# Kernel tuning notes

Measured on AMD Instinct MI355X. Metric: run time of the kernel, lower is better.

## Reference

```python
import jax, jax.numpy as jnp
import numpy as np

NI, ND, NH = 64, 64, 4
NB, NLOC, NNEI = 4, 2048, 64


def setup_inputs() -> dict:
    key = jax.random.key(0)
    ks = jax.random.split(key, 7)
    g1 = jax.random.normal(ks[0], (NB, NLOC, NI), dtype=jnp.float32)
    gg1 = jax.random.normal(ks[1], (NB, NLOC, NNEI, NI), dtype=jnp.float32)
    nlist_mask = jax.random.randint(ks[2], (NB, NLOC, NNEI), 0, 2).astype(bool)
    # torch Linear weight (out, in); store transposed for x @ W
    Wq = jax.random.normal(ks[3], (NI, ND * NH), dtype=jnp.float32) * (1.0 / np.sqrt(NI))
    Wkv = jax.random.normal(ks[4], (NI, (ND + NI) * NH), dtype=jnp.float32) * (1.0 / np.sqrt(NI))
    Wh = jax.random.normal(ks[5], (NI * NH, NI), dtype=jnp.float32) * (1.0 / np.sqrt(NI * NH))
    bh = jax.random.normal(ks[6], (NI,), dtype=jnp.float32) * 0.01
    return {"g1": g1, "gg1": gg1, "nlist_mask": nlist_mask,
            "Wq": Wq, "Wkv": Wkv, "Wh": Wh, "bh": bh}


def reference(g1, gg1, nlist_mask, Wq, Wkv, Wh, bh):
    nb, nloc, nnei = nlist_mask.shape
    ni, nd, nh = NI, ND, NH
    # q: (nb, nloc, nh, nd)
    q = (g1 @ Wq).reshape(nb, nloc, nd, nh).transpose(0, 1, 3, 2)
    # kv: (nb, nloc, nnei, nd, 2*nh) -> (nb, nloc, 2*nh, nnei, nd); valid since ni == nd
    kv = (gg1 @ Wkv).reshape(nb, nloc, nnei, nd, 2 * nh).transpose(0, 1, 4, 2, 3)
    k = kv[:, :, :nh]          # (nb, nloc, nh, nnei, nd)
    v = kv[:, :, nh:2 * nh]    # (nb, nloc, nh, nnei, nd)
    attnw = jnp.einsum('blhd,blhjd->blhj', q, k) / np.sqrt(nd).astype(np.float32)
    m = nlist_mask[:, :, None, :]  # (nb, nloc, 1, nnei)
    attnw = jnp.where(m, attnw, -jnp.inf)
    attnw = jax.nn.softmax(attnw, axis=-1)
    attnw = jnp.where(m, attnw, 0.0)
    ret = jnp.einsum('blhj,blhjd->blhd', attnw, v).reshape(nb, nloc, nh * ni)
    return ret @ Wh + bh
```

## Files before the change

kernel.cpp:

```cpp
#include <hip/hip_runtime.h>
#include <hip/hip_fp16.h>
#include <math.h>

#define NATOM 8192

namespace {

typedef _Float16 half8 __attribute__((ext_vector_type(8)));
typedef _Float16 half2t __attribute__((ext_vector_type(2)));
typedef float f32x4 __attribute__((ext_vector_type(4)));

__global__ void pack_weights(const float* __restrict__ Wkv,
                             const float* __restrict__ Wq,
                             const float* __restrict__ Wh,
                             _Float16* __restrict__ out) {
  int tid = blockIdx.x * 256 + threadIdx.x;
  if (tid < 32768) {
    int i = tid >> 9, c = tid & 511;
    int ks = i >> 5, jj = i & 7, lqk = (i >> 3) & 3;
    int d = c >> 3, e = c & 7, isv = e >> 2, h = e & 3;
    int T = isv * 16 + (d >> 2);
    int m = ((d & 3) << 2) | h;
    int l = lqk * 16 + m;
    out[(((T * 2 + ks) * 64) + l) * 8 + jj] = (_Float16)Wkv[i * 512 + c];
  } else if (tid < 49152) {
    int idx = tid - 32768;
    int i = idx >> 8, c = idx & 255;
    out[32768 + c * 64 + i] = (_Float16)Wq[i * 256 + c];
  } else {
    int idx = tid - 49152;
    int k = idx >> 6, c = idx & 63;
    out[49152 + c * 256 + k] = (_Float16)Wh[k * 64 + c];
  }
}

__device__ __forceinline__ float dot8(half8 a, half8 b, float acc) {
  acc = __builtin_amdgcn_fdot2((half2t){a[0], a[1]}, (half2t){b[0], b[1]}, acc, false);
  acc = __builtin_amdgcn_fdot2((half2t){a[2], a[3]}, (half2t){b[2], b[3]}, acc, false);
  acc = __builtin_amdgcn_fdot2((half2t){a[4], a[5]}, (half2t){b[4], b[5]}, acc, false);
  acc = __builtin_amdgcn_fdot2((half2t){a[6], a[7]}, (half2t){b[6], b[7]}, acc, false);
  return acc;
}

__global__ __launch_bounds__(256, 4)
void local_atten_kernel(const float* __restrict__ g1,
                        const float* __restrict__ gg1,
                        const int* __restrict__ mask,
                        const _Float16* __restrict__ wpack,
                        const float* __restrict__ bh,
                        float* __restrict__ out) {
  __shared__ __align__(16) __half gs[64 * 64];
  __shared__ __align__(16) __half g1h[64];
  __shared__ __align__(16) unsigned char blob[3072];
  __shared__ __align__(8) __half aws2[64][4];
  __shared__ __align__(16) __half rets[256];

  float* qs = reinterpret_cast<float*>(blob);
  __half (*sred)[4][64] = reinterpret_cast<__half(*)[4][64]>(blob + 1024);
  float (*redbuf)[64] = reinterpret_cast<float(*)[64]>(blob);

  const _Float16* wkvp = wpack;
  const _Float16* wqp  = wpack + 32768;
  const _Float16* whp  = wpack + 49152;

  const int t = threadIdx.x;
  const int lane = t & 63;
  const int wave = t >> 6;
  const int lq = lane >> 4;
  const int lr = lane & 15;
  const int atom = blockIdx.x;

  if (t < 64) g1h[t] = __float2half(g1[(size_t)atom * 64 + t]);

  {
    const float4* src = reinterpret_cast<const float4*>(gg1 + (size_t)atom * 4096);
#pragma unroll
    for (int r = 0; r < 4; ++r) {
      int idx4 = t + 256 * r;
      int j = idx4 >> 4;
      int i4 = (idx4 & 15) << 2;
      float4 v = src[idx4];
      __half2 h01 = __floats2half2_rn(v.x, v.y);
      __half2 h23 = __floats2half2_rn(v.z, v.w);
      int g = i4 >> 3;
      int addr = j * 64 + ((g ^ (j & 7)) << 3) + (i4 & 7);
      union { __half2 h[2]; uint2 u; } pk;
      pk.h[0] = h01; pk.h[1] = h23;
      *reinterpret_cast<uint2*>(&gs[addr]) = pk.u;
    }
  }
  __syncthreads();

  half8 bfrag[4][2];
  {
    const __half* bp0 = &gs[lr * 64 + ((lq ^ (lr & 7)) << 3)];
    const __half* bp1 = &gs[lr * 64 + (((4 + lq) ^ (lr & 7)) << 3)];
#pragma unroll
    for (int jt = 0; jt < 4; ++jt) {
      bfrag[jt][0] = *reinterpret_cast<const half8*>(bp0 + jt * 1024);
      bfrag[jt][1] = *reinterpret_cast<const half8*>(bp1 + jt * 1024);
    }
  }

  const half8* ap_base = reinterpret_cast<const half8*>(wkvp);
  half8 a0 = ap_base[(wave * 4) * 128 + lane];
  half8 a1 = ap_base[(wave * 4) * 128 + 64 + lane];

  {
    float qacc = 0.f;
    const half8* wrow = reinterpret_cast<const half8*>(wqp + t * 64);
    const half8* grow = reinterpret_cast<const half8*>(&g1h[0]);
#pragma unroll
    for (int ks = 0; ks < 8; ++ks) qacc = dot8(wrow[ks], grow[ks], qacc);
    qs[t] = qacc;
  }
  __syncthreads();

  float sacc[4][4];
#pragma unroll
  for (int jt = 0; jt < 4; ++jt)
#pragma unroll
    for (int h = 0; h < 4; ++h) sacc[jt][h] = 0.f;

#pragma unroll
  for (int it = 0; it < 4; ++it) {
    const int T = wave * 4 + it;
    const int Tn = (it < 3) ? (T + 1) : (16 + wave * 4);
    half8 na0 = ap_base[Tn * 128 + lane];
    half8 na1 = ap_base[Tn * 128 + 64 + lane];

    const int d = T * 4 + lq;
    float4 q4 = *reinterpret_cast<const float4*>(&qs[d * 4]);
#pragma unroll
    for (int jt = 0; jt < 4; ++jt) {
      f32x4 acc = {0.f, 0.f, 0.f, 0.f};
      acc = __builtin_amdgcn_mfma_f32_16x16x32_f16(a0, bfrag[jt][0], acc, 0, 0, 0);
      acc = __builtin_amdgcn_mfma_f32_16x16x32_f16(a1, bfrag[jt][1], acc, 0, 0, 0);
      sacc[jt][0] = fmaf(acc[0], q4.x, sacc[jt][0]);
      sacc[jt][1] = fmaf(acc[1], q4.y, sacc[jt][1]);
      sacc[jt][2] = fmaf(acc[2], q4.z, sacc[jt][2]);
      sacc[jt][3] = fmaf(acc[3], q4.w, sacc[jt][3]);
    }
    a0 = na0; a1 = na1;
  }

  const int mreg = mask[(size_t)atom * 64 + lane];

#pragma unroll
  for (int jt = 0; jt < 4; ++jt)
#pragma unroll
    for (int h = 0; h < 4; ++h) {
      sacc[jt][h] += __shfl_xor(sacc[jt][h], 16);
      sacc[jt][h] += __shfl_xor(sacc[jt][h], 32);
    }
  if (lq == 0) {
#pragma unroll
    for (int h = 0; h < 4; ++h)
#pragma unroll
      for (int jt = 0; jt < 4; ++jt)
        sred[wave][h][jt * 16 + lr] = __float2half(sacc[jt][h]);
  }
  __syncthreads();

  {
    float s = __half2float(sred[0][wave][lane]) + __half2float(sred[1][wave][lane]) +
              __half2float(sred[2][wave][lane]) + __half2float(sred[3][wave][lane]);
    s *= 0.125f;
    s = mreg ? s : -INFINITY;
    float mx = s;
#pragma unroll
    for (int off = 32; off > 0; off >>= 1) mx = fmaxf(mx, __shfl_xor(mx, off));
    float pe = mreg ? __expf(s - mx) : 0.f;
    float sum = pe;
#pragma unroll
    for (int off = 32; off > 0; off >>= 1) sum += __shfl_xor(sum, off);
    float aw = (sum > 0.f) ? (pe / sum) : 0.f;
    aws2[lane][wave] = __float2half(aw);
  }
  __syncthreads();

  float awf[4][4];
#pragma unroll
  for (int jt = 0; jt < 4; ++jt) {
    union { uint2 u; __half2 h[2]; } awu;
    awu.u = *reinterpret_cast<const uint2*>(&aws2[jt * 16 + lr][0]);
    float2 f01 = __half22float2(awu.h[0]);
    float2 f23 = __half22float2(awu.h[1]);
    awf[jt][0] = f01.x; awf[jt][1] = f01.y; awf[jt][2] = f23.x; awf[jt][3] = f23.y;
  }

#pragma unroll
  for (int it = 0; it < 4; ++it) {
    const int T = 16 + wave * 4 + it;
    half8 na0 = a0, na1 = a1;
    if (it < 3) {
      na0 = ap_base[(T + 1) * 128 + lane];
      na1 = ap_base[(T + 1) * 128 + 64 + lane];
    }
    float part[4] = {0.f, 0.f, 0.f, 0.f};
#pragma unroll
    for (int jt = 0; jt < 4; ++jt) {
      f32x4 acc = {0.f, 0.f, 0.f, 0.f};
      acc = __builtin_amdgcn_mfma_f32_16x16x32_f16(a0, bfrag[jt][0], acc, 0, 0, 0);
      acc = __builtin_amdgcn_mfma_f32_16x16x32_f16(a1, bfrag[jt][1], acc, 0, 0, 0);
      part[0] = fmaf(acc[0], awf[jt][0], part[0]);
      part[1] = fmaf(acc[1], awf[jt][1], part[1]);
      part[2] = fmaf(acc[2], awf[jt][2], part[2]);
      part[3] = fmaf(acc[3], awf[jt][3], part[3]);
    }
#pragma unroll
    for (int r = 0; r < 4; ++r) {
      part[r] += __shfl_xor(part[r], 1);
      part[r] += __shfl_xor(part[r], 2);
      part[r] += __shfl_xor(part[r], 4);
      part[r] += __shfl_xor(part[r], 8);
    }
    if (lr == 0) {
      const int d = (T - 16) * 4 + lq;
#pragma unroll
      for (int r = 0; r < 4; ++r) rets[r * 64 + d] = __float2half(part[r]);
    }
    a0 = na0; a1 = na1;
  }
  __syncthreads();

  {
    float part = 0.f;
    const half8* wrow = reinterpret_cast<const half8*>(whp + lane * 256 + wave * 64);
    const half8* rrow = reinterpret_cast<const half8*>(&rets[wave * 64]);
#pragma unroll
    for (int ks = 0; ks < 8; ++ks) part = dot8(wrow[ks], rrow[ks], part);
    redbuf[wave][lane] = part;
  }
  __syncthreads();
  if (t < 64)
    out[(size_t)atom * 64 + t] =
        redbuf[0][t] + redbuf[1][t] + redbuf[2][t] + redbuf[3][t] + bh[t];
}

}

extern "C" void kernel_launch(void* const* d_in, const int* in_sizes, int n_in,
                              void* d_out, int out_size, void* d_ws, size_t ws_size,
                              hipStream_t stream) {
  const float* g1   = (const float*)d_in[0];
  const float* gg1  = (const float*)d_in[1];
  const int*   mask = (const int*)d_in[2];
  const float* Wq   = (const float*)d_in[3];
  const float* Wkv  = (const float*)d_in[4];
  const float* Wh   = (const float*)d_in[5];
  const float* bh   = (const float*)d_in[6];
  float* out = (float*)d_out;
  (void)in_sizes; (void)n_in; (void)ws_size; (void)out_size;

  _Float16* wpack = (_Float16*)d_ws;
  pack_weights<<<256, 256, 0, stream>>>(Wkv, Wq, Wh, wpack);
  local_atten_kernel<<<NATOM, 256, 0, stream>>>(g1, gg1, mask, wpack, bh, out);
}
```

Before: 280.3 us.

## Assign one atom per wave to eliminate block-level barriers

Each wave now handles a whole atom, with per-wave shared buffers, instead of four waves splitting one atom's work. This removes all __syncthreads and the cross-wave shared-memory reductions, and keeps the softmax in registers using shuffles. In exchange each wave loops over all 32 weight tiles, so more weight traffic reaches each wave from L2, register pressure rises (launch bounds lowered to 2), and the grid has a quarter as many blocks.

```diff
diff --git a/kernel.cpp b/kernel.cpp
--- a/kernel.cpp
+++ b/kernel.cpp
@@ -42,22 +42,17 @@
   return acc;
 }
 
-__global__ __launch_bounds__(256, 4)
+__global__ __launch_bounds__(256, 2)
 void local_atten_kernel(const float* __restrict__ g1,
                         const float* __restrict__ gg1,
                         const int* __restrict__ mask,
                         const _Float16* __restrict__ wpack,
                         const float* __restrict__ bh,
                         float* __restrict__ out) {
-  __shared__ __align__(16) __half gs[64 * 64];
-  __shared__ __align__(16) __half g1h[64];
-  __shared__ __align__(16) unsigned char blob[3072];
-  __shared__ __align__(8) __half aws2[64][4];
-  __shared__ __align__(16) __half rets[256];
-
-  float* qs = reinterpret_cast<float*>(blob);
-  __half (*sred)[4][64] = reinterpret_cast<__half(*)[4][64]>(blob + 1024);
-  float (*redbuf)[64] = reinterpret_cast<float(*)[64]>(blob);
+  __shared__ __align__(16) __half gs[4][4096];
+  __shared__ __align__(16) float  qs[4][256];
+  __shared__ __align__(16) __half rets[4][256];
+  __shared__ __align__(16) __half g1s[4][64];
 
   const _Float16* wkvp = wpack;
   const _Float16* wqp  = wpack + 32768;
@@ -68,33 +63,65 @@
   const int wave = t >> 6;
   const int lq = lane >> 4;
   const int lr = lane & 15;
-  const int atom = blockIdx.x;
-
-  if (t < 64) g1h[t] = __float2half(g1[(size_t)atom * 64 + t]);
+  const int atom = blockIdx.x * 4 + wave;
+
+  __half* gsw  = gs[wave];
+  float*  qsw  = qs[wave];
+  __half* retw = rets[wave];
+  __half* g1w  = g1s[wave];
+
+  int mreg[4];
+#pragma unroll
+  for (int jt = 0; jt < 4; ++jt)
+    mreg[jt] = mask[(size_t)atom * 64 + jt * 16 + lr];
+
+  const half8* ap_base = reinterpret_cast<const half8*>(wkvp);
+  half8 a0 = ap_base[lane];
+  half8 a1 = ap_base[64 + lane];
+
+  g1w[lane] = __float2half(g1[(size_t)atom * 64 + lane]);
 
   {
     const float4* src = reinterpret_cast<const float4*>(gg1 + (size_t)atom * 4096);
 #pragma unroll
-    for (int r = 0; r < 4; ++r) {
-      int idx4 = t + 256 * r;
-      int j = idx4 >> 4;
-      int i4 = (idx4 & 15) << 2;
-      float4 v = src[idx4];
-      __half2 h01 = __floats2half2_rn(v.x, v.y);
-      __half2 h23 = __floats2half2_rn(v.z, v.w);
-      int g = i4 >> 3;
-      int addr = j * 64 + ((g ^ (j & 7)) << 3) + (i4 & 7);
-      union { __half2 h[2]; uint2 u; } pk;
-      pk.h[0] = h01; pk.h[1] = h23;
-      *reinterpret_cast<uint2*>(&gs[addr]) = pk.u;
-    }
-  }
-  __syncthreads();
+    for (int bat = 0; bat < 2; ++bat) {
+      float4 v[8];
+#pragma unroll
+      for (int r = 0; r < 8; ++r) v[r] = src[lane + 64 * (bat * 8 + r)];
+#pragma unroll
+      for (int r = 0; r < 8; ++r) {
+        int idx4 = lane + 64 * (bat * 8 + r);
+        int j = idx4 >> 4;
+        int i4 = (idx4 & 15) << 2;
+        __half2 h01 = __floats2half2_rn(v[r].x, v[r].y);
+        __half2 h23 = __floats2half2_rn(v[r].z, v[r].w);
+        int g = i4 >> 3;
+        int addr = j * 64 + ((g ^ (j & 7)) << 3) + (i4 & 7);
+        union { __half2 h[2]; uint2 u; } pk;
+        pk.h[0] = h01; pk.h[1] = h23;
+        *reinterpret_cast<uint2*>(&gsw[addr]) = pk.u;
+      }
+    }
+  }
+
+  {
+    const half8* grow = reinterpret_cast<const half8*>(g1w);
+    float4 qv;
+#pragma unroll
+    for (int cc = 0; cc < 4; ++cc) {
+      const half8* wrow = reinterpret_cast<const half8*>(wqp + (lane * 4 + cc) * 64);
+      float qacc = 0.f;
+#pragma unroll
+      for (int ks = 0; ks < 8; ++ks) qacc = dot8(wrow[ks], grow[ks], qacc);
+      qv[cc] = qacc;
+    }
+    *reinterpret_cast<float4*>(&qsw[lane * 4]) = qv;
+  }
 
   half8 bfrag[4][2];
   {
-    const __half* bp0 = &gs[lr * 64 + ((lq ^ (lr & 7)) << 3)];
-    const __half* bp1 = &gs[lr * 64 + (((4 + lq) ^ (lr & 7)) << 3)];
+    const __half* bp0 = &gsw[lr * 64 + ((lq ^ (lr & 7)) << 3)];
+    const __half* bp1 = &gsw[lr * 64 + (((4 + lq) ^ (lr & 7)) << 3)];
 #pragma unroll
     for (int jt = 0; jt < 4; ++jt) {
       bfrag[jt][0] = *reinterpret_cast<const half8*>(bp0 + jt * 1024);
@@ -102,20 +129,6 @@
     }
   }
 
-  const half8* ap_base = reinterpret_cast<const half8*>(wkvp);
-  half8 a0 = ap_base[(wave * 4) * 128 + lane];
-  half8 a1 = ap_base[(wave * 4) * 128 + 64 + lane];
-
-  {
-    float qacc = 0.f;
-    const half8* wrow = reinterpret_cast<const half8*>(wqp + t * 64);
-    const half8* grow = reinterpret_cast<const half8*>(&g1h[0]);
-#pragma unroll
-    for (int ks = 0; ks < 8; ++ks) qacc = dot8(wrow[ks], grow[ks], qacc);
-    qs[t] = qacc;
-  }
-  __syncthreads();
-
   float sacc[4][4];
 #pragma unroll
   for (int jt = 0; jt < 4; ++jt)
@@ -123,14 +136,11 @@
     for (int h = 0; h < 4; ++h) sacc[jt][h] = 0.f;
 
 #pragma unroll
-  for (int it = 0; it < 4; ++it) {
-    const int T = wave * 4 + it;
-    const int Tn = (it < 3) ? (T + 1) : (16 + wave * 4);
-    half8 na0 = ap_base[Tn * 128 + lane];
-    half8 na1 = ap_base[Tn * 128 + 64 + lane];
-
+  for (int T = 0; T < 16; ++T) {
+    half8 na0 = ap_base[(T + 1) * 128 + lane];
+    half8 na1 = ap_base[(T + 1) * 128 + 64 + lane];
     const int d = T * 4 + lq;
-    float4 q4 = *reinterpret_cast<const float4*>(&qs[d * 4]);
+    float4 q4 = *reinterpret_cast<const float4*>(&qsw[d * 4]);
 #pragma unroll
     for (int jt = 0; jt < 4; ++jt) {
       f32x4 acc = {0.f, 0.f, 0.f, 0.f};
@@ -144,8 +154,6 @@
     a0 = na0; a1 = na1;
   }
 
-  const int mreg = mask[(size_t)atom * 64 + lane];
-
 #pragma unroll
   for (int jt = 0; jt < 4; ++jt)
 #pragma unroll
@@ -153,47 +161,37 @@
       sacc[jt][h] += __shfl_xor(sacc[jt][h], 16);
       sacc[jt][h] += __shfl_xor(sacc[jt][h], 32);
     }
-  if (lq == 0) {
-#pragma unroll
-    for (int h = 0; h < 4; ++h)
-#pragma unroll
-      for (int jt = 0; jt < 4; ++jt)
-        sred[wave][h][jt * 16 + lr] = __float2half(sacc[jt][h]);
-  }
-  __syncthreads();
-
-  {
-    float s = __half2float(sred[0][wave][lane]) + __half2float(sred[1][wave][lane]) +
-              __half2float(sred[2][wave][lane]) + __half2float(sred[3][wave][lane]);
-    s *= 0.125f;
-    s = mreg ? s : -INFINITY;
-    float mx = s;
-#pragma unroll
-    for (int off = 32; off > 0; off >>= 1) mx = fmaxf(mx, __shfl_xor(mx, off));
-    float pe = mreg ? __expf(s - mx) : 0.f;
-    float sum = pe;
-#pragma unroll
-    for (int off = 32; off > 0; off >>= 1) sum += __shfl_xor(sum, off);
-    float aw = (sum > 0.f) ? (pe / sum) : 0.f;
-    aws2[lane][wave] = __float2half(aw);
-  }
-  __syncthreads();
-
-  float awf[4][4];
-#pragma unroll
-  for (int jt = 0; jt < 4; ++jt) {
-    union { uint2 u; __half2 h[2]; } awu;
-    awu.u = *reinterpret_cast<const uint2*>(&aws2[jt * 16 + lr][0]);
-    float2 f01 = __half22float2(awu.h[0]);
-    float2 f23 = __half22float2(awu.h[1]);
-    awf[jt][0] = f01.x; awf[jt][1] = f01.y; awf[jt][2] = f23.x; awf[jt][3] = f23.y;
-  }
-
-#pragma unroll
-  for (int it = 0; it < 4; ++it) {
-    const int T = 16 + wave * 4 + it;
+
+  float aw[4][4];
+  {
+#pragma unroll
+    for (int jt = 0; jt < 4; ++jt)
+#pragma unroll
+      for (int h = 0; h < 4; ++h)
+        sacc[jt][h] = mreg[jt] ? sacc[jt][h] * 0.125f : -INFINITY;
+#pragma unroll
+    for (int h = 0; h < 4; ++h) {
+      float mx = fmaxf(fmaxf(sacc[0][h], sacc[1][h]), fmaxf(sacc[2][h], sacc[3][h]));
+#pragma unroll
+      for (int off = 8; off > 0; off >>= 1) mx = fmaxf(mx, __shfl_xor(mx, off));
+      float p0 = mreg[0] ? __expf(sacc[0][h] - mx) : 0.f;
+      float p1 = mreg[1] ? __expf(sacc[1][h] - mx) : 0.f;
+      float p2 = mreg[2] ? __expf(sacc[2][h] - mx) : 0.f;
+      float p3 = mreg[3] ? __expf(sacc[3][h] - mx) : 0.f;
+      float sum = p0 + p1 + p2 + p3;
+#pragma unroll
+      for (int off = 8; off > 0; off >>= 1) sum += __shfl_xor(sum, off);
+      float inv = (sum > 0.f) ? (1.f / sum) : 0.f;
+      aw[0][h] = p0 * inv; aw[1][h] = p1 * inv;
+      aw[2][h] = p2 * inv; aw[3][h] = p3 * inv;
+    }
+  }
+
+#pragma unroll
+  for (int Ti = 0; Ti < 16; ++Ti) {
+    const int T = 16 + Ti;
     half8 na0 = a0, na1 = a1;
-    if (it < 3) {
+    if (Ti < 15) {
       na0 = ap_base[(T + 1) * 128 + lane];
       na1 = ap_base[(T + 1) * 128 + 64 + lane];
     }
@@ -203,10 +201,10 @@
       f32x4 acc = {0.f, 0.f, 0.f, 0.f};
       acc = __builtin_amdgcn_mfma_f32_16x16x32_f16(a0, bfrag[jt][0], acc, 0, 0, 0);
       acc = __builtin_amdgcn_mfma_f32_16x16x32_f16(a1, bfrag[jt][1], acc, 0, 0, 0);
-      part[0] = fmaf(acc[0], awf[jt][0], part[0]);
-      part[1] = fmaf(acc[1], awf[jt][1], part[1]);
-      part[2] = fmaf(acc[2], awf[jt][2], part[2]);
-      part[3] = fmaf(acc[3], awf[jt][3], part[3]);
+      part[0] = fmaf(acc[0], aw[jt][0], part[0]);
+      part[1] = fmaf(acc[1], aw[jt][1], part[1]);
+      part[2] = fmaf(acc[2], aw[jt][2], part[2]);
+      part[3] = fmaf(acc[3], aw[jt][3], part[3]);
     }
 #pragma unroll
     for (int r = 0; r < 4; ++r) {
@@ -216,26 +214,24 @@
       part[r] += __shfl_xor(part[r], 8);
     }
     if (lr == 0) {
-      const int d = (T - 16) * 4 + lq;
-#pragma unroll
-      for (int r = 0; r < 4; ++r) rets[r * 64 + d] = __float2half(part[r]);
+      const int d = Ti * 4 + lq;
+#pragma unroll
+      for (int r = 0; r < 4; ++r) retw[r * 64 + d] = __float2half(part[r]);
     }
     a0 = na0; a1 = na1;
   }
-  __syncthreads();
-
-  {
-    float part = 0.f;
-    const half8* wrow = reinterpret_cast<const half8*>(whp + lane * 256 + wave * 64);
-    const half8* rrow = reinterpret_cast<const half8*>(&rets[wave * 64]);
-#pragma unroll
-    for (int ks = 0; ks < 8; ++ks) part = dot8(wrow[ks], rrow[ks], part);
-    redbuf[wave][lane] = part;
-  }
-  __syncthreads();
-  if (t < 64)
-    out[(size_t)atom * 64 + t] =
-        redbuf[0][t] + redbuf[1][t] + redbuf[2][t] + redbuf[3][t] + bh[t];
+
+  {
+    const half8* wrow = reinterpret_cast<const half8*>(whp + lane * 256);
+    const half8* rrow = reinterpret_cast<const half8*>(retw);
+    float o0 = 0.f, o1 = 0.f;
+#pragma unroll
+    for (int ks = 0; ks < 16; ++ks) {
+      o0 = dot8(wrow[ks], rrow[ks], o0);
+      o1 = dot8(wrow[16 + ks], rrow[16 + ks], o1);
+    }
+    out[(size_t)atom * 64 + lane] = o0 + o1 + bh[lane];
+  }
 }
 
 }
@@ -255,5 +251,5 @@
 
   _Float16* wpack = (_Float16*)d_ws;
   pack_weights<<<256, 256, 0, stream>>>(Wkv, Wq, Wh, wpack);
-  local_atten_kernel<<<NATOM, 256, 0, stream>>>(g1, gg1, mask, wpack, bh, out);
-}
+  local_atten_kernel<<<NATOM / 4, 256, 0, stream>>>(g1, gg1, mask, wpack, bh, out);
+}
```

Measured after the change: 280.4 us. No clear change (+0.0%).
